# Kernel tuning notes

Hardware: AMD Instinct MI355X
Metric: run time of the kernel (lower is better)

The kernel has to match this reference:

```python
import jax, jax.numpy as jnp
import numpy as np

SCALE = 16.0
IGNORE_THRESH = 0.5
BAD_CONF_WEIGHT = 1.25
NUM_CLASSES = 4
ANCHORS_PX = np.array([[16,16],[32,32],[64,64],[128,128],[256,256],[32,64],[64,32],[128,64],[64,128]], dtype=np.float32)


def _bce_logits(x, z):
    # stable binary_cross_entropy_with_logits, elementwise
    return jnp.maximum(x, 0.0) - x * z + jnp.log1p(jnp.exp(-jnp.abs(x)))


def _inv_tanh(y):
    mid = 0.5 * jnp.log((1.0 + y) / (1.0 - y))
    return jnp.where(y <= -1.0, -2.0, jnp.where(y >= 1.0, 2.0, mid))


def _iou_cxcywh(box1, box2):
    # matches bbox_iou(x1y1x2y2=False): (cx, cy, half_w, half_h) with +1 area convention
    b1x1, b1x2 = box1[:, 0] - box1[:, 2], box1[:, 0] + box1[:, 2]
    b1y1, b1y2 = box1[:, 1] - box1[:, 3], box1[:, 1] + box1[:, 3]
    b2x1, b2x2 = box2[:, 0] - box2[:, 2], box2[:, 0] + box2[:, 2]
    b2y1, b2y2 = box2[:, 1] - box2[:, 3], box2[:, 1] + box2[:, 3]
    iw = jnp.clip(jnp.minimum(b1x2, b2x2) - jnp.maximum(b1x1, b2x1) + 1.0, 0.0)
    ih = jnp.clip(jnp.minimum(b1y2, b2y2) - jnp.maximum(b1y1, b2y1) + 1.0, 0.0)
    inter = iw * ih
    a1 = (b1x2 - b1x1 + 1.0) * (b1y2 - b1y1 + 1.0)
    a2 = (b2x2 - b2x1 + 1.0) * (b2y2 - b2y1 + 1.0)
    return inter / (a1 + a2 - inter + 1e-16)


def _yolo_loss(prediction, target, target_sizes):
    nB, nA, nH, nW = prediction.shape[:4]
    nC = NUM_CLASSES
    anchors = jnp.asarray(ANCHORS_PX) / SCALE  # grid units, [nA,2]
    x = prediction[..., 1]
    y = prediction[..., 2]
    w = prediction[..., 5]
    h = prediction[..., 4]
    pred_conf = prediction[..., 0]
    pred_cls = prediction[..., 6:]
    grid_x = jnp.arange(nW, dtype=jnp.float32)[None, None, None, :]
    grid_y = jnp.arange(nH, dtype=jnp.float32)[None, None, :, None]
    aw4 = anchors[:, 0][None, :, None, None]
    ah4 = anchors[:, 1][None, :, None, None]
    xd, yd, wd, hd = map(jax.lax.stop_gradient, (x, y, w, h))  # torch uses .data
    pred_boxes = jnp.stack([
        jnp.tanh(xd) + 0.5 + grid_x + 0.0 * yd,
        jnp.tanh(yd) + 0.5 + grid_y + 0.0 * xd,
        jnp.exp(wd) * aw4,
        jnp.exp(hd) * ah4,
    ], axis=-1)  # [nB,nA,nH,nW,4]

    # target[:, :, [0,1,3,4]] /= scale (targets are constants w.r.t. grad)
    col_scale = jnp.ones(target.shape[-1], jnp.float32).at[jnp.array([0, 1, 3, 4])].set(1.0 / SCALE)
    tgt = jax.lax.stop_gradient(target) * col_scale

    pred_conf_sg = jax.lax.stop_gradient(pred_conf)
    pred_cls_sg = jax.lax.stop_gradient(pred_cls)
    b_idx = jnp.arange(nB)
    a_idx = jnp.arange(nA)
    awv = anchors[:, 0]
    ahv = anchors[:, 1]
    anchor_area = (awv + 1.0) * (ahv + 1.0)
    T = tgt.shape[1]
    ts_arr = target_sizes.astype(jnp.int32)
    zeros = jnp.zeros((nB, nA, nH, nW), jnp.float32)
    carry0 = dict(mask=zeros, conf_mask=jnp.ones_like(zeros), tx=zeros, ty=zeros, tw=zeros,
                  th=zeros, tconf=zeros, tcls=jnp.zeros((nB, nA, nH, nW, nC), jnp.float32),
                  nGT=jnp.zeros((), jnp.int32), nCorrect=jnp.zeros((), jnp.int32))

    def step(c, xs):
        t, row = xs  # row: [nB, 13+nC]
        gx, gy, gh_, gw_ = row[:, 0], row[:, 1], row[:, 3], row[:, 4]
        valid = (t < ts_arr) & (gw_ != 0) & (gh_ != 0)
        gi = jnp.clip(gx.astype(jnp.int32), 0, nW - 1)
        gj = jnp.clip(gy.astype(jnp.int32), 0, nH - 1)
        # anchor IoU (boxes [0,0,w,h] as corners, +1 convention) -> [nB,nA]
        inter = (jnp.minimum(gw_[:, None], awv[None, :]) + 1.0) * (jnp.minimum(gh_[:, None], ahv[None, :]) + 1.0)
        anch_ious = inter / ((gw_ + 1.0)[:, None] * (gh_ + 1.0)[:, None] + anchor_area[None, :] - inter + 1e-16)
        ii = (b_idx[:, None], a_idx[None, :], gj[:, None], gi[:, None])
        cm = c['conf_mask']
        cm = cm.at[ii].set(jnp.where(valid[:, None] & (anch_ious > IGNORE_THRESH), 0.0, cm[ii]))
        best_n = jnp.argmax(anch_ious, axis=1)
        idx = (b_idx, best_n, gj, gi)

        def setv(A, val):
            return A.at[idx].set(jnp.where(valid, val, A[idx]))

        mask = setv(c['mask'], 1.0)
        cm = setv(cm, 1.0)
        tx_ = setv(c['tx'], _inv_tanh(gx - (gi.astype(jnp.float32) + 0.5)))
        ty_ = setv(c['ty'], _inv_tanh(gy - (gj.astype(jnp.float32) + 0.5)))
        tw_ = setv(c['tw'], jnp.log(gw_ / awv[best_n] + 1e-16))
        th_ = setv(c['th'], jnp.log(gh_ / ahv[best_n] + 1e-16))
        tconf_ = setv(c['tconf'], 1.0)
        cls_row = row[:, 13:]
        tcls_ = c['tcls'].at[idx].set(jnp.where(valid[:, None], cls_row, c['tcls'][idx]))
        nGT = c['nGT'] + valid.sum().astype(jnp.int32)
        pb = pred_boxes[idx]  # [nB,4]
        iou = _iou_cxcywh(jnp.stack([gx, gy, gw_, gh_], axis=1), pb)
        plabel = jnp.argmax(pred_cls_sg[idx], axis=-1)
        score = pred_conf_sg[idx]
        correct = valid & (iou > 0.5) & (plabel == jnp.argmax(cls_row, axis=-1)) & (score > 0)
        nCorrect = c['nCorrect'] + correct.sum().astype(jnp.int32)
        return dict(mask=mask, conf_mask=cm, tx=tx_, ty=ty_, tw=tw_, th=th_, tconf=tconf_,
                    tcls=tcls_, nGT=nGT, nCorrect=nCorrect), None

    carry, _ = jax.lax.scan(step, carry0, (jnp.arange(T, dtype=jnp.int32), jnp.swapaxes(tgt, 0, 1)))

    mask = carry['mask']
    conf_mask = carry['conf_mask']
    cmf = conf_mask - mask  # conf_mask_false

    def masked_mean(v, m):
        return jnp.sum(v * m) / jnp.maximum(jnp.sum(m), 1.0)

    loss_conf = BAD_CONF_WEIGHT * masked_mean(_bce_logits(pred_conf, carry['tconf']), cmf)
    loss_x = masked_mean((x - carry['tx']) ** 2, mask)
    loss_y = masked_mean((y - carry['ty']) ** 2, mask)
    loss_w = masked_mean((w - carry['tw']) ** 2, mask)
    loss_h = masked_mean((h - carry['th']) ** 2, mask)
    labels = jnp.argmax(carry['tcls'], axis=-1)  # [nB,nA,nH,nW]
    ce = jax.nn.logsumexp(pred_cls, axis=-1) - jnp.take_along_axis(pred_cls, labels[..., None], axis=-1)[..., 0]
    loss_cls = masked_mean(ce, mask) / nB
    loss_conf = loss_conf + masked_mean(_bce_logits(pred_conf, carry['tconf']), mask)
    loss = loss_x + loss_y + loss_w + loss_h + loss_conf + loss_cls

    nGT = carry['nGT'].astype(jnp.float32)
    nCorrect = carry['nCorrect'].astype(jnp.float32)
    nProposals = jnp.sum(pred_conf_sg > 0).astype(jnp.float32)
    recall = jnp.where(nGT > 0, nCorrect / jnp.maximum(nGT, 1.0), 1.0)
    precision = jnp.where(nProposals > 0, nCorrect / jnp.maximum(nProposals, 1.0), 1.0)
    return loss, loss_x + loss_y + loss_w + loss_h, loss_conf, loss_cls, recall, precision


def setup_inputs() -> dict:
    key = jax.random.key(0)
    ks = jax.random.split(key, 7)
    nB, nA, nH, nW, nC, T = 16, 9, 128, 128, NUM_CLASSES, 50
    prediction = jax.random.normal(ks[0], (nB, nA, nH, nW, 6 + nC), dtype=jnp.float32)
    gx = jax.random.uniform(ks[1], (nB, T), dtype=jnp.float32) * (nW * SCALE)
    gy = jax.random.uniform(ks[2], (nB, T), dtype=jnp.float32) * (nH * SCALE)
    gh = jax.random.uniform(ks[3], (nB, T), dtype=jnp.float32) * 180.0 + 12.0
    gw = jax.random.uniform(ks[4], (nB, T), dtype=jnp.float32) * 180.0 + 12.0
    cls_idx = jax.random.randint(ks[5], (nB, T), 0, nC)
    target = jnp.zeros((nB, T, 13 + nC), jnp.float32)
    target = target.at[..., 0].set(gx).at[..., 1].set(gy).at[..., 3].set(gh).at[..., 4].set(gw)
    target = target.at[..., 13:].set(jax.nn.one_hot(cls_idx, nC, dtype=jnp.float32))
    target_sizes = jax.random.randint(ks[6], (nB,), 10, T + 1)
    return {"prediction": prediction, "target": target, "target_sizes": target_sizes}


def reference(prediction, target, target_sizes):
    return _yolo_loss(prediction, target, target_sizes)
```

## Files before the change

kernel.cpp:

```cpp
#include <hip/hip_runtime.h>
#include <math.h>

static constexpr int NA = 9;
static constexpr int NH = 128;
static constexpr int NW = 128;
static constexpr int NC = 4;
static constexpr int CH = 6 + NC;
static constexpr int TCOLS = 13 + NC;
static constexpr float SCALE_INV = 1.0f / 16.0f;
static constexpr int NBG = 2048;
static constexpr int SCAN_STRIDE = 16;

__constant__ float c_aw[NA] = {1.f, 2.f, 4.f, 8.f, 16.f, 2.f, 4.f, 8.f, 4.f};
__constant__ float c_ah[NA] = {1.f, 2.f, 4.f, 8.f, 16.f, 4.f, 2.f, 4.f, 8.f};

static constexpr int NSLOT = 11;

__device__ __forceinline__ float bcef(float x, float z) {
    return fmaxf(x, 0.f) - x * z + log1pf(expf(-fabsf(x)));
}
__device__ __forceinline__ float invtanh(float y) {
    if (y <= -1.f) return -2.f;
    if (y >= 1.f) return 2.f;
    return 0.5f * logf((1.f + y) / (1.f - y));
}
__device__ __forceinline__ float wredf(float v) {
#pragma unroll
    for (int o = 32; o; o >>= 1) v += __shfl_down(v, o, 64);
    return v;
}

template <int TT>
__global__ __launch_bounds__(256) void k_scan(const float* __restrict__ pred,
                                              const float* __restrict__ tgt,
                                              const int* __restrict__ tsz,
                                              float* __restrict__ scanPart, int T) {
    const int b = blockIdx.x;
    const int tid = threadIdx.x;
    const int lane = tid & 63;
    const int wave = tid >> 6;

    __shared__ int sPack[64];
    __shared__ float sAccW[4][NSLOT];

    const int ts = tsz[b];
    if (tid < 64) sPack[tid] = 0;
    __syncthreads();

    float rTx = 0.f, rTy = 0.f, rTw = 0.f, rTh = 0.f;
    int rTl = 0;
    float fGT = 0.f, fCor = 0.f;

    if (wave == 0 && lane < T) {
        const int t = lane;
        const float* row = tgt + (size_t)(b * T + t) * TCOLS;
        float gx = row[0] * SCALE_INV, gy = row[1] * SCALE_INV;
        float gh = row[3] * SCALE_INV, gw = row[4] * SCALE_INV;
        int valid = (t < ts) && (gw != 0.f) && (gh != 0.f);
        int gi = (int)gx; gi = gi < 0 ? 0 : (gi > NW - 1 ? NW - 1 : gi);
        int gj = (int)gy; gj = gj < 0 ? 0 : (gj > NH - 1 ? NH - 1 : gj);

        float bestIou = -1.f; int best = 0; int ign = 0;
#pragma unroll
        for (int a = 0; a < NA; a++) {
            float aw = c_aw[a], ah = c_ah[a];
            float inter = (fminf(gw, aw) + 1.f) * (fminf(gh, ah) + 1.f);
            float uni = (gw + 1.f) * (gh + 1.f) + (aw + 1.f) * (ah + 1.f) - inter + 1e-16f;
            float iou = inter / uni;
            if (iou > 0.5f) ign |= (1 << a);
            if (iou > bestIou) { bestIou = iou; best = a; }
        }
        sPack[t] = (valid ? 1 : 0) | (best << 1) | (ign << 5) | ((gj * NW + gi) << 14);
        rTx = invtanh(gx - ((float)gi + 0.5f));
        rTy = invtanh(gy - ((float)gj + 0.5f));
        rTw = logf(gw / c_aw[best] + 1e-16f);
        rTh = logf(gh / c_ah[best] + 1e-16f);

        float cc0 = row[13], cc1 = row[14], cc2 = row[15], cc3 = row[16];
        rTl = 0; float cmax = cc0;
        if (cc1 > cmax) { cmax = cc1; rTl = 1; }
        if (cc2 > cmax) { cmax = cc2; rTl = 2; }
        if (cc3 > cmax) { cmax = cc3; rTl = 3; }

        if (valid) {
            fGT = 1.f;
            const float* p = pred + ((((size_t)b * NA + best) * NH + gj) * NW + gi) * CH;
            float p0 = p[0];
            float px = tanhf(p[1]) + 0.5f + (float)gi;
            float py = tanhf(p[2]) + 0.5f + (float)gj;
            float pw = expf(p[5]) * c_aw[best];
            float ph = expf(p[4]) * c_ah[best];
            float b1x1 = gx - gw, b1x2 = gx + gw, b1y1 = gy - gh, b1y2 = gy + gh;
            float b2x1 = px - pw, b2x2 = px + pw, b2y1 = py - ph, b2y2 = py + ph;
            float iw = fmaxf(fminf(b1x2, b2x2) - fmaxf(b1x1, b2x1) + 1.f, 0.f);
            float ih = fmaxf(fminf(b1y2, b2y2) - fmaxf(b1y1, b2y1) + 1.f, 0.f);
            float inter = iw * ih;
            float a1 = (b1x2 - b1x1 + 1.f) * (b1y2 - b1y1 + 1.f);
            float a2 = (b2x2 - b2x1 + 1.f) * (b2y2 - b2y1 + 1.f);
            float iou = inter / (a1 + a2 - inter + 1e-16f);
            float q0 = p[6], q1 = p[7], q2 = p[8], q3 = p[9];
            int pl = 0; float qm = q0;
            if (q1 > qm) { qm = q1; pl = 1; }
            if (q2 > qm) { qm = q2; pl = 2; }
            if (q3 > qm) { qm = q3; pl = 3; }
            if (iou > 0.5f && pl == rTl && p0 > 0.f) fCor = 1.f;
        }
    }
    __syncthreads();

    const int pk = sPack[lane];

    float corrNum = 0.f, corrDen = 0.f, lconfM = 0.f, maskCnt = 0.f;
#pragma unroll
    for (int ai = 0; ai < 3; ai++) {
        const int a = wave + 4 * ai;
        if (a >= NA) break;
        int valid = pk & 1;
        int myCell = pk >> 14;
        int myBest = (pk >> 1) & 0xF;
        int isBest = valid && (myBest == a);
        int isIgn = valid && !isBest && ((pk >> (5 + a)) & 1);
        int myPri = isBest ? (2 * lane + 1) : (isIgn ? (2 * lane) : -2);
        int maxPri = -1, anyBest = 0;
#pragma unroll
        for (int u = 0; u < TT; u++) {
            int q = __shfl(pk, u, 64);
            int same = (q & 1) && ((q >> 14) == myCell);
            int qb = (q >> 1) & 0xF;
            int qBest = same && (qb == a);
            int qIgn = same && (qb != a) && ((q >> (5 + a)) & 1);
            int pri = qBest ? (2 * u + 1) : (qIgn ? (2 * u) : -1);
            maxPri = max(maxPri, pri);
            anyBest |= qBest;
        }
        if (valid && myPri >= 0 && myPri == maxPri) {
            int gj = myCell >> 7, gi = myCell & (NW - 1);
            float conf = pred[((((size_t)b * NA + a) * NH + gj) * NW + gi) * CH];
            float bce0 = bcef(conf, 0.f);
            if (anyBest) {
                float cm = (maxPri & 1) ? 1.f : 0.f;
                float cmf = cm - 1.f;
                float bce1 = bcef(conf, 1.f);
                corrNum += bce1 * cmf - bce0;
                corrDen += cmf - 1.f;
                lconfM += bce1;
                maskCnt += 1.f;
            } else {
                corrNum -= bce0;
                corrDen -= 1.f;
            }
        }
    }

    float lx = 0.f, ly = 0.f, lw = 0.f, lh = 0.f, lcls = 0.f;
    if (wave == 3) {
        int valid = pk & 1;
        int myCell = pk >> 14, myBest = (pk >> 1) & 0xF;
        int isLast = valid;
#pragma unroll
        for (int u = 0; u < TT; u++) {
            int q = __shfl(pk, u, 64);
            int later = (u > lane) && (q & 1) && ((q >> 14) == myCell) &&
                        (((q >> 1) & 0xF) == myBest);
            isLast &= !later;
        }
        if (isLast) {
            int gj = myCell >> 7, gi = myCell & (NW - 1);
            const float* pp = pred + ((((size_t)b * NA + myBest) * NH + gj) * NW + gi) * CH;
            const float* row = tgt + (size_t)(b * T + lane) * TCOLS;
            float gx = row[0] * SCALE_INV, gy = row[1] * SCALE_INV;
            float gh_ = row[3] * SCALE_INV, gw_ = row[4] * SCALE_INV;
            float tx = invtanh(gx - ((float)gi + 0.5f));
            float ty = invtanh(gy - ((float)gj + 0.5f));
            float tw = logf(gw_ / c_aw[myBest] + 1e-16f);
            float th = logf(gh_ / c_ah[myBest] + 1e-16f);
            float cc0 = row[13], cc1 = row[14], cc2 = row[15], cc3 = row[16];
            int tl = 0; float cmax = cc0;
            if (cc1 > cmax) { cmax = cc1; tl = 1; }
            if (cc2 > cmax) { cmax = cc2; tl = 2; }
            if (cc3 > cmax) { cmax = cc3; tl = 3; }
            float dx = pp[1] - tx, dy = pp[2] - ty;
            float dw = pp[5] - tw, dh = pp[4] - th;
            lx = dx * dx; ly = dy * dy; lw = dw * dw; lh = dh * dh;
            float q0 = pp[6], q1 = pp[7], q2 = pp[8], q3 = pp[9];
            float m = fmaxf(fmaxf(q0, q1), fmaxf(q2, q3));
            float lse = m + logf(expf(q0 - m) + expf(q1 - m) + expf(q2 - m) + expf(q3 - m));
            lcls = lse - pp[6 + tl];
        }
    }

    float v;
    v = wredf(corrNum); if (lane == 0) sAccW[wave][0] = v;
    v = wredf(corrDen); if (lane == 0) sAccW[wave][1] = v;
    v = wredf(maskCnt); if (lane == 0) sAccW[wave][2] = v;
    v = wredf(lx);      if (lane == 0) sAccW[wave][3] = v;
    v = wredf(ly);      if (lane == 0) sAccW[wave][4] = v;
    v = wredf(lw);      if (lane == 0) sAccW[wave][5] = v;
    v = wredf(lh);      if (lane == 0) sAccW[wave][6] = v;
    v = wredf(lcls);    if (lane == 0) sAccW[wave][7] = v;
    v = wredf(lconfM);  if (lane == 0) sAccW[wave][8] = v;
    v = wredf(fGT);     if (lane == 0) sAccW[wave][9] = v;
    v = wredf(fCor);    if (lane == 0) sAccW[wave][10] = v;
    __syncthreads();
    if (tid < NSLOT) {
        float s = sAccW[0][tid] + sAccW[1][tid] + sAccW[2][tid] + sAccW[3][tid];
        scanPart[b * SCAN_STRIDE + tid] = s;
    }
}

__global__ __launch_bounds__(256) void k_bg(const float* __restrict__ pred,
                                            float2* __restrict__ bgPart, int nCells) {
    __shared__ float sdat[2][4];
    float s0 = 0.f, npos = 0.f;
    const int stride = gridDim.x * blockDim.x;
#pragma unroll 4
    for (int c = blockIdx.x * blockDim.x + threadIdx.x; c < nCells; c += stride) {
        float cv = __builtin_nontemporal_load(&pred[(size_t)c * CH]);
        s0 += fmaxf(cv, 0.f) + log1pf(expf(-fabsf(cv)));
        npos += (cv > 0.f) ? 1.f : 0.f;
    }
    s0 = wredf(s0); npos = wredf(npos);
    int wid = threadIdx.x >> 6;
    if ((threadIdx.x & 63) == 0) { sdat[0][wid] = s0; sdat[1][wid] = npos; }
    __syncthreads();
    if (threadIdx.x == 0) {
        float a0 = sdat[0][0] + sdat[0][1] + sdat[0][2] + sdat[0][3];
        float a1 = sdat[1][0] + sdat[1][1] + sdat[1][2] + sdat[1][3];
        bgPart[blockIdx.x] = make_float2(a0, a1);
    }
}

__global__ __launch_bounds__(256) void k_fin(const float* __restrict__ scanPart,
                                             const float2* __restrict__ bgPart,
                                             float* __restrict__ out,
                                             double totalCells, int nB, int nbg) {
    __shared__ double sred[2][4];
    __shared__ double sscan[NSLOT];
    const int tid = threadIdx.x;

    double s0 = 0.0, np = 0.0;
    for (int i = tid; i < nbg; i += 256) {
        float2 v = bgPart[i];
        s0 += (double)v.x; np += (double)v.y;
    }
#pragma unroll
    for (int o = 32; o; o >>= 1) {
        s0 += __shfl_down(s0, o, 64);
        np += __shfl_down(np, o, 64);
    }
    int wid = tid >> 6;
    if ((tid & 63) == 0) { sred[0][wid] = s0; sred[1][wid] = np; }
    if (tid < NSLOT) {
        double s = 0.0;
        for (int b = 0; b < nB; b++) s += (double)scanPart[b * SCAN_STRIDE + tid];
        sscan[tid] = s;
    }
    __syncthreads();
    if (tid == 0) {
        double S0 = sred[0][0] + sred[0][1] + sred[0][2] + sred[0][3];
        double nProp = sred[1][0] + sred[1][1] + sred[1][2] + sred[1][3];
        double corrNum = sscan[0], corrDen = sscan[1], maskCnt = sscan[2];
        double lx = sscan[3], ly = sscan[4], lw = sscan[5], lh = sscan[6];
        double lcls = sscan[7], lconfM = sscan[8], nGT = sscan[9], nCor = sscan[10];

        double msum = fmax(maskCnt, 1.0);
        double cden = fmax(totalCells + corrDen, 1.0);
        double loss_conf = 1.25 * (S0 + corrNum) / cden + lconfM / msum;
        double lx_ = lx / msum, ly_ = ly / msum, lw_ = lw / msum, lh_ = lh / msum;
        double lcls_ = (lcls / msum) / (double)nB;
        double coord = lx_ + ly_ + lw_ + lh_;
        double loss = coord + loss_conf + lcls_;
        double recall = (nGT > 0.0) ? nCor / fmax(nGT, 1.0) : 1.0;
        double precision = (nProp > 0.0) ? nCor / fmax(nProp, 1.0) : 1.0;

        out[0] = (float)loss;
        out[1] = (float)coord;
        out[2] = (float)loss_conf;
        out[3] = (float)lcls_;
        out[4] = (float)recall;
        out[5] = (float)precision;
    }
}

extern "C" void kernel_launch(void* const* d_in, const int* in_sizes, int n_in,
                              void* d_out, int out_size, void* d_ws, size_t ws_size,
                              hipStream_t stream) {
    const float* pred = (const float*)d_in[0];
    const float* tgt = (const float*)d_in[1];
    const int* tsz = (const int*)d_in[2];
    int nB = in_sizes[2];
    int T = in_sizes[1] / (nB * TCOLS);
    long long total = (long long)nB * NA * NH * NW;
    int nCells = (int)total;

    float* scanPart = (float*)d_ws;
    float2* bgPart = (float2*)((char*)d_ws + (size_t)nB * SCAN_STRIDE * sizeof(float));
    float* out = (float*)d_out;

    hipLaunchKernelGGL(k_bg, dim3(NBG), dim3(256), 0, stream, pred, bgPart, nCells);
    hipLaunchKernelGGL(k_scan<64>, dim3(nB), dim3(256), 0, stream, pred, tgt, tsz,
                       scanPart, T);
    hipLaunchKernelGGL(k_fin, dim3(1), dim3(256), 0, stream, scanPart, bgPart, out,
                       (double)total, nB, NBG);
}
```

Measured before the change: 46.71 us.

## Replace O(T^2) shuffle dedup in k_scan with shared-memory hash of cells

The per-target pairwise shuffle loops that resolved which target owns each (cell, anchor) are replaced by a shared-memory open-addressing hash of occupied cells, with atomicMax used to pick the winning priority and best target per slot. Confidence and box/class losses are then computed in one pass over hash slots, with target regressions staged in shared memory. This removes the 64-iteration shuffle loops and the duplicate target reloads in the last wave, at the cost of shared-memory atomics, extra barriers and a CAS probing loop. k_scan runs on only nB blocks and k_bg likely dominates the total time, so the effect on overall time is probably small.

Measured after the change: 37.76 us. 19.1% less time.

```diff
diff --git a/kernel.cpp b/kernel.cpp
--- a/kernel.cpp
+++ b/kernel.cpp
@@ -10,6 +10,7 @@
 static constexpr float SCALE_INV = 1.0f / 16.0f;
 static constexpr int NBG = 2048;
 static constexpr int SCAN_STRIDE = 16;
+static constexpr int HSLOTS = 128;
 
 __constant__ float c_aw[NA] = {1.f, 2.f, 4.f, 8.f, 16.f, 2.f, 4.f, 8.f, 4.f};
 __constant__ float c_ah[NA] = {1.f, 2.f, 4.f, 8.f, 16.f, 4.f, 2.f, 4.f, 8.f};
@@ -30,7 +31,6 @@
     return v;
 }
 
-template <int TT>
 __global__ __launch_bounds__(256) void k_scan(const float* __restrict__ pred,
                                               const float* __restrict__ tgt,
                                               const int* __restrict__ tsz,
@@ -40,15 +40,17 @@
     const int lane = tid & 63;
     const int wave = tid >> 6;
 
-    __shared__ int sPack[64];
+    __shared__ int sPack[64], sTl[64], sSlot[64];
+    __shared__ float sTx[64], sTy[64], sTw[64], sTh[64];
+    __shared__ int sKey[HSLOTS];
+    __shared__ int sPri[HSLOTS * NA];
+    __shared__ int sBest[HSLOTS * NA];
     __shared__ float sAccW[4][NSLOT];
 
+    for (int i = tid; i < HSLOTS; i += 256) sKey[i] = -1;
+    for (int i = tid; i < HSLOTS * NA; i += 256) { sPri[i] = -1; sBest[i] = -1; }
+
     const int ts = tsz[b];
-    if (tid < 64) sPack[tid] = 0;
-    __syncthreads();
-
-    float rTx = 0.f, rTy = 0.f, rTw = 0.f, rTh = 0.f;
-    int rTl = 0;
     float fGT = 0.f, fCor = 0.f;
 
     if (wave == 0 && lane < T) {
@@ -71,16 +73,17 @@
             if (iou > bestIou) { bestIou = iou; best = a; }
         }
         sPack[t] = (valid ? 1 : 0) | (best << 1) | (ign << 5) | ((gj * NW + gi) << 14);
-        rTx = invtanh(gx - ((float)gi + 0.5f));
-        rTy = invtanh(gy - ((float)gj + 0.5f));
-        rTw = logf(gw / c_aw[best] + 1e-16f);
-        rTh = logf(gh / c_ah[best] + 1e-16f);
+        sTx[t] = invtanh(gx - ((float)gi + 0.5f));
+        sTy[t] = invtanh(gy - ((float)gj + 0.5f));
+        sTw[t] = logf(gw / c_aw[best] + 1e-16f);
+        sTh[t] = logf(gh / c_ah[best] + 1e-16f);
 
         float cc0 = row[13], cc1 = row[14], cc2 = row[15], cc3 = row[16];
-        rTl = 0; float cmax = cc0;
-        if (cc1 > cmax) { cmax = cc1; rTl = 1; }
-        if (cc2 > cmax) { cmax = cc2; rTl = 2; }
-        if (cc3 > cmax) { cmax = cc3; rTl = 3; }
+        int tl = 0; float cmax = cc0;
+        if (cc1 > cmax) { cmax = cc1; tl = 1; }
+        if (cc2 > cmax) { cmax = cc2; tl = 2; }
+        if (cc3 > cmax) { cmax = cc3; tl = 3; }
+        sTl[t] = tl;
 
         if (valid) {
             fGT = 1.f;
@@ -103,89 +106,72 @@
             if (q1 > qm) { qm = q1; pl = 1; }
             if (q2 > qm) { qm = q2; pl = 2; }
             if (q3 > qm) { qm = q3; pl = 3; }
-            if (iou > 0.5f && pl == rTl && p0 > 0.f) fCor = 1.f;
-        }
-    }
-    __syncthreads();
-
-    const int pk = sPack[lane];
+            if (iou > 0.5f && pl == tl && p0 > 0.f) fCor = 1.f;
+        }
+    }
+    __syncthreads();
+
+    if (tid < T) {
+        int p = sPack[tid];
+        if (p & 1) {
+            int cell = p >> 14;
+            int slot = cell & (HSLOTS - 1);
+            while (true) {
+                int old = atomicCAS(&sKey[slot], -1, cell);
+                if (old == -1 || old == cell) break;
+                slot = (slot + 1) & (HSLOTS - 1);
+            }
+            sSlot[tid] = slot;
+        }
+    }
+    __syncthreads();
+
+    for (int item = tid; item < T * NA; item += 256) {
+        int t = item / NA, a = item - t * NA;
+        int p = sPack[t];
+        if (!(p & 1)) continue;
+        int slot = sSlot[t];
+        int best = (p >> 1) & 0xF;
+        if (a == best) {
+            atomicMax(&sPri[slot * NA + a], 2 * t + 1);
+            atomicMax(&sBest[slot * NA + a], 2 * t + 1);
+        } else if ((p >> (5 + a)) & 1) {
+            atomicMax(&sPri[slot * NA + a], 2 * t);
+        }
+    }
+    __syncthreads();
 
     float corrNum = 0.f, corrDen = 0.f, lconfM = 0.f, maskCnt = 0.f;
-#pragma unroll
-    for (int ai = 0; ai < 3; ai++) {
-        const int a = wave + 4 * ai;
-        if (a >= NA) break;
-        int valid = pk & 1;
-        int myCell = pk >> 14;
-        int myBest = (pk >> 1) & 0xF;
-        int isBest = valid && (myBest == a);
-        int isIgn = valid && !isBest && ((pk >> (5 + a)) & 1);
-        int myPri = isBest ? (2 * lane + 1) : (isIgn ? (2 * lane) : -2);
-        int maxPri = -1, anyBest = 0;
-#pragma unroll
-        for (int u = 0; u < TT; u++) {
-            int q = __shfl(pk, u, 64);
-            int same = (q & 1) && ((q >> 14) == myCell);
-            int qb = (q >> 1) & 0xF;
-            int qBest = same && (qb == a);
-            int qIgn = same && (qb != a) && ((q >> (5 + a)) & 1);
-            int pri = qBest ? (2 * u + 1) : (qIgn ? (2 * u) : -1);
-            maxPri = max(maxPri, pri);
-            anyBest |= qBest;
-        }
-        if (valid && myPri >= 0 && myPri == maxPri) {
-            int gj = myCell >> 7, gi = myCell & (NW - 1);
-            float conf = pred[((((size_t)b * NA + a) * NH + gj) * NW + gi) * CH];
-            float bce0 = bcef(conf, 0.f);
-            if (anyBest) {
-                float cm = (maxPri & 1) ? 1.f : 0.f;
-                float cmf = cm - 1.f;
-                float bce1 = bcef(conf, 1.f);
-                corrNum += bce1 * cmf - bce0;
-                corrDen += cmf - 1.f;
-                lconfM += bce1;
-                maskCnt += 1.f;
-            } else {
-                corrNum -= bce0;
-                corrDen -= 1.f;
-            }
-        }
-    }
-
     float lx = 0.f, ly = 0.f, lw = 0.f, lh = 0.f, lcls = 0.f;
-    if (wave == 3) {
-        int valid = pk & 1;
-        int myCell = pk >> 14, myBest = (pk >> 1) & 0xF;
-        int isLast = valid;
-#pragma unroll
-        for (int u = 0; u < TT; u++) {
-            int q = __shfl(pk, u, 64);
-            int later = (u > lane) && (q & 1) && ((q >> 14) == myCell) &&
-                        (((q >> 1) & 0xF) == myBest);
-            isLast &= !later;
-        }
-        if (isLast) {
-            int gj = myCell >> 7, gi = myCell & (NW - 1);
-            const float* pp = pred + ((((size_t)b * NA + myBest) * NH + gj) * NW + gi) * CH;
-            const float* row = tgt + (size_t)(b * T + lane) * TCOLS;
-            float gx = row[0] * SCALE_INV, gy = row[1] * SCALE_INV;
-            float gh_ = row[3] * SCALE_INV, gw_ = row[4] * SCALE_INV;
-            float tx = invtanh(gx - ((float)gi + 0.5f));
-            float ty = invtanh(gy - ((float)gj + 0.5f));
-            float tw = logf(gw_ / c_aw[myBest] + 1e-16f);
-            float th = logf(gh_ / c_ah[myBest] + 1e-16f);
-            float cc0 = row[13], cc1 = row[14], cc2 = row[15], cc3 = row[16];
-            int tl = 0; float cmax = cc0;
-            if (cc1 > cmax) { cmax = cc1; tl = 1; }
-            if (cc2 > cmax) { cmax = cc2; tl = 2; }
-            if (cc3 > cmax) { cmax = cc3; tl = 3; }
-            float dx = pp[1] - tx, dy = pp[2] - ty;
-            float dw = pp[5] - tw, dh = pp[4] - th;
-            lx = dx * dx; ly = dy * dy; lw = dw * dw; lh = dh * dh;
+    for (int it = tid; it < HSLOTS * NA; it += 256) {
+        int slot = it / NA, a = it - slot * NA;
+        int cell = sKey[slot];
+        if (cell < 0) continue;
+        int pm = sPri[it];
+        if (pm < 0) continue;
+        int bm = sBest[it];
+        const float* pp = pred + ((size_t)(b * NA + a) * (NH * NW) + cell) * CH;
+        float conf = pp[0];
+        float bce0 = bcef(conf, 0.f);
+        if (bm >= 0) {
+            float cm = (float)(pm & 1);
+            float cmf = cm - 1.f;
+            float bce1 = bcef(conf, 1.f);
+            corrNum += bce1 * cmf - bce0;
+            corrDen += cmf - 1.f;
+            lconfM += bce1;
+            maskCnt += 1.f;
+            int t = bm >> 1;
+            float dx = pp[1] - sTx[t], dy = pp[2] - sTy[t];
+            float dw = pp[5] - sTw[t], dh = pp[4] - sTh[t];
+            lx += dx * dx; ly += dy * dy; lw += dw * dw; lh += dh * dh;
             float q0 = pp[6], q1 = pp[7], q2 = pp[8], q3 = pp[9];
             float m = fmaxf(fmaxf(q0, q1), fmaxf(q2, q3));
             float lse = m + logf(expf(q0 - m) + expf(q1 - m) + expf(q2 - m) + expf(q3 - m));
-            lcls = lse - pp[6 + tl];
+            lcls += lse - pp[6 + sTl[t]];
+        } else {
+            corrNum -= bce0;
+            corrDen -= 1.f;
         }
     }
 
@@ -298,7 +284,7 @@
     float* out = (float*)d_out;
 
     hipLaunchKernelGGL(k_bg, dim3(NBG), dim3(256), 0, stream, pred, bgPart, nCells);
-    hipLaunchKernelGGL(k_scan<64>, dim3(nB), dim3(256), 0, stream, pred, tgt, tsz,
+    hipLaunchKernelGGL(k_scan, dim3(nB), dim3(256), 0, stream, pred, tgt, tsz,
                        scanPart, T);
     hipLaunchKernelGGL(k_fin, dim3(1), dim3(256), 0, stream, scanPart, bgPart, out,
                        (double)total, nB, NBG);
```
